# Performance work log

Hardware: AMD Instinct MI355X
Metric: run time of the kernel (lower is better)

Reference implementation:

```python
import jax, jax.numpy as jnp
import numpy as np

GRAPH_SIZES = [864, 1728, 3456, 6912]
VERTEX_NUM = 6890
B, NZ, FC_DIM = 128, 128, 512
CH = [128, 128, 64, 32, 16]
EDGE_FACTOR = 6  # directed edges per node (triangle mesh)
LRELU = 0.2


def setup_inputs() -> dict:
    key = jax.random.key(0)
    ks = jax.random.split(key, 24)
    s = 0.02
    inp = {
        'x': jax.random.normal(ks[0], (B, NZ), jnp.float32),
        'fc_w1': s * jax.random.normal(ks[1], (NZ, FC_DIM), jnp.float32),
        'fc_b1': jnp.zeros((FC_DIM,), jnp.float32),
        'fc_w2': s * jax.random.normal(ks[2], (FC_DIM, GRAPH_SIZES[0] * CH[0]), jnp.float32),
        'fc_b2': jnp.zeros((GRAPH_SIZES[0] * CH[0],), jnp.float32),
    }
    # Chebyshev weights [K=3, C_in, C_out] per layer (+ final conv to 3)
    cio = [(CH[0], CH[1]), (CH[1], CH[2]), (CH[2], CH[3]), (CH[3], CH[4]), (CH[4], 3)]
    for i, (ci, co) in enumerate(cio):
        inp[f'W{i}'] = s * jax.random.normal(ks[3 + i], (3, ci, co), jnp.float32)
        inp[f'b{i}'] = jnp.zeros((co,), jnp.float32)
    # fixed edge lists per level
    for i, n in enumerate(GRAPH_SIZES):
        e = EDGE_FACTOR * n
        inp[f'edge{i}'] = jax.random.randint(ks[10 + i], (2, e), 0, n, dtype=jnp.int64)
    inp['perm_back'] = jax.random.randint(ks[20], (GRAPH_SIZES[-1],), 0, GRAPH_SIZES[-1], dtype=jnp.int64)
    return inp


def cheb_conv(x, edge_index, W, b, num_nodes):
    # PyG-style ChebConv with lambda_max=2: L_hat = L - I = -D^{-1/2} A D^{-1/2}
    src, dst = edge_index[0], edge_index[1]
    deg = jnp.zeros((num_nodes,), x.dtype).at[dst].add(jnp.ones(src.shape, x.dtype))
    dinv = jnp.where(deg > 0, 1.0 / jnp.sqrt(jnp.maximum(deg, 1.0)), 0.0)
    norm = -(dinv[src] * dinv[dst])  # [E]

    def prop(h):  # h: [B, N, C] -> L_hat @ h (gather + scatter-add over edges)
        msg = h[:, src, :] * norm[None, :, None]
        return jnp.zeros_like(h).at[:, dst, :].add(msg)

    Tx0 = x
    Tx1 = prop(Tx0)
    Tx2 = 2.0 * prop(Tx1) - Tx0
    out = (jnp.einsum('bnc,co->bno', Tx0, W[0])
           + jnp.einsum('bnc,co->bno', Tx1, W[1])
           + jnp.einsum('bnc,co->bno', Tx2, W[2]))
    return out + b


def lrelu(x):
    return jnp.where(x >= 0, x, LRELU * x)


def reference(x, fc_w1, fc_b1, fc_w2, fc_b2,
              W0, b0, W1, b1, W2, b2, W3, b3, W4, b4,
              edge0, edge1, edge2, edge3, perm_back):
    h = jax.nn.relu(x @ fc_w1 + fc_b1)
    h = h @ fc_w2 + fc_b2                      # dropout = identity (eval mode)
    h = h.reshape(h.shape[0], GRAPH_SIZES[0], -1)  # [B, 864, 128]
    edges = [edge0, edge1, edge2, edge3]
    Ws = [(W0, b0), (W1, b1), (W2, b2), (W3, b3)]
    for i in range(4):
        h = lrelu(cheb_conv(h, edges[i], Ws[i][0], Ws[i][1], GRAPH_SIZES[i]))
        if i < 3:
            h = jnp.repeat(h, 2, axis=1)       # Upsample(scale_factor=2) along nodes
    h = cheb_conv(h, edge3, W4, b4, GRAPH_SIZES[3])  # final conv to 3 coords
    h = h[:, perm_back, :]                      # perm_data gather
    return h[:, :VERTEX_NUM, :]
```

## Files before the change

### kernel.cpp

```cpp
#include <hip/hip_runtime.h>
#include <hip/hip_bf16.h>

#define DEVFN __device__ __forceinline__

__global__ void k_signal(float* out, float v) {
    if (threadIdx.x == 0 && blockIdx.x == 0) out[0] = v;
}

__global__ void k_detect64(const long long* __restrict__ p, int count, int* flag) {
    if (threadIdx.x == 0 && blockIdx.x == 0) {
        int ok = 1;
        for (int i = 0; i < count; i++) {
            long long v = p[i];
            if (v < 0 || v >= (1LL << 30)) { ok = 0; break; }
        }
        *flag = ok;
    }
}

__global__ __launch_bounds__(256) void k_cvt_idx(const void* __restrict__ p, int n,
                                                 const int* __restrict__ flag,
                                                 int* __restrict__ out) {
    int i = blockIdx.x * 256 + threadIdx.x;
    if (i >= n) return;
    if (*flag) out[i] = (int)((const long long*)p)[i];
    else       out[i] = ((const int*)p)[i];
}

__global__ __launch_bounds__(256) void k_fc1(const float* __restrict__ x,
                                             const float* __restrict__ w,
                                             const float* __restrict__ b,
                                             float* __restrict__ out) {
    int j = blockIdx.x * 256 + threadIdx.x;
    int m = blockIdx.y;
    float acc = b[j];
    const float* xr = x + m * 128;
    for (int k = 0; k < 128; k++)
        acc = fmaf(xr[k], w[k * 512 + j], acc);
    out[m * 512 + j] = fmaxf(acc, 0.f);
}

__global__ __launch_bounds__(256) void k_fc2_gemm3(const float* __restrict__ h1,
                                                   const float* __restrict__ w,
                                                   const float* __restrict__ bias,
                                                   float* __restrict__ out) {
    const int N = 110592, K = 512;
    constexpr int KT = 32, MT = 128, NT = 64, AST = 37;
    __shared__ float At[MT * AST];
    __shared__ float Bt[KT * NT];

    const int tid = threadIdx.x;
    const int cg = tid & 7;
    const int rg = tid >> 3;
    const int nbase = blockIdx.x * NT;
    const int c0 = cg * 8;

    float acc[4][8];
#pragma unroll
    for (int jj = 0; jj < 8; jj++) {
        float bj = bias[nbase + c0 + jj];
#pragma unroll
        for (int r = 0; r < 4; r++) acc[r][jj] = bj;
    }

    for (int k0 = 0; k0 < K; k0 += KT) {
        __syncthreads();
#pragma unroll
        for (int it = 0; it < 4; it++) {
            int idx = tid + it * 256;
            int row = idx >> 3, k4 = (idx & 7) * 4;
            float4 a = *(const float4*)(h1 + row * K + k0 + k4);
            float* dst = At + row * AST + k4;
            dst[0] = a.x; dst[1] = a.y; dst[2] = a.z; dst[3] = a.w;
        }
#pragma unroll
        for (int it = 0; it < 2; it++) {
            int idx = tid + it * 256;
            int kk = idx >> 4, c4 = (idx & 15) * 4;
            *(float4*)(Bt + kk * NT + c4) =
                *(const float4*)(w + (size_t)(k0 + kk) * N + nbase + c4);
        }
        __syncthreads();
#pragma unroll 4
        for (int k = 0; k < KT; k++) {
            float a0 = At[(rg * 4 + 0) * AST + k];
            float a1 = At[(rg * 4 + 1) * AST + k];
            float a2 = At[(rg * 4 + 2) * AST + k];
            float a3 = At[(rg * 4 + 3) * AST + k];
            float4 w0 = *(const float4*)(Bt + k * NT + c0);
            float4 w1 = *(const float4*)(Bt + k * NT + c0 + 4);
            float wv[8] = {w0.x, w0.y, w0.z, w0.w, w1.x, w1.y, w1.z, w1.w};
#pragma unroll
            for (int jj = 0; jj < 8; jj++) {
                acc[0][jj] = fmaf(a0, wv[jj], acc[0][jj]);
                acc[1][jj] = fmaf(a1, wv[jj], acc[1][jj]);
                acc[2][jj] = fmaf(a2, wv[jj], acc[2][jj]);
                acc[3][jj] = fmaf(a3, wv[jj], acc[3][jj]);
            }
        }
    }
#pragma unroll
    for (int r = 0; r < 4; r++) {
        int m = rg * 4 + r;
        float4 o0 = {acc[r][0], acc[r][1], acc[r][2], acc[r][3]};
        float4 o1 = {acc[r][4], acc[r][5], acc[r][6], acc[r][7]};
        *(float4*)(out + (size_t)m * N + nbase + c0) = o0;
        *(float4*)(out + (size_t)m * N + nbase + c0 + 4) = o1;
    }
}

__global__ __launch_bounds__(256) void k_zero_int(int* p, int n) {
    int i = blockIdx.x * 256 + threadIdx.x;
    if (i < n) p[i] = 0;
}

__global__ __launch_bounds__(256) void k_deg(const int* __restrict__ dst, int e,
                                             int* __restrict__ deg) {
    int i = blockIdx.x * 256 + threadIdx.x;
    if (i < e) atomicAdd(&deg[dst[i]], 1);
}

__global__ __launch_bounds__(256) void k_dinv(const int* __restrict__ deg,
                                              float* __restrict__ dinv, int n) {
    int i = blockIdx.x * 256 + threadIdx.x;
    if (i < n) dinv[i] = deg[i] > 0 ? 1.0f / sqrtf((float)deg[i]) : 0.0f;
}

__global__ __launch_bounds__(256) void k_scan(const int* __restrict__ deg,
                                              int* __restrict__ row_ptr, int n) {
    __shared__ int part[256];
    int tid = threadIdx.x;
    int per = (n + 255) / 256;
    int start = tid * per;
    int end = min(start + per, n);
    int s = 0;
    for (int i = start; i < end; i++) s += deg[i];
    part[tid] = s;
    __syncthreads();
    for (int off = 1; off < 256; off <<= 1) {
        int t = (tid >= off) ? part[tid - off] : 0;
        __syncthreads();
        part[tid] += t;
        __syncthreads();
    }
    int base = (tid == 0) ? 0 : part[tid - 1];
    int run = base;
    for (int i = start; i < end; i++) { row_ptr[i] = run; run += deg[i]; }
    if (tid == 255) row_ptr[n] = part[255];
}

__global__ __launch_bounds__(256) void k_fill(const int* __restrict__ src,
                                              const int* __restrict__ dst, int e,
                                              const int* __restrict__ row_ptr,
                                              int* __restrict__ cnt,
                                              const float* __restrict__ dinv,
                                              int* __restrict__ col, float* __restrict__ val) {
    int i = blockIdx.x * 256 + threadIdx.x;
    if (i >= e) return;
    int d = dst[i], s = src[i];
    int slot = row_ptr[d] + atomicAdd(&cnt[d], 1);
    col[slot] = s;
    val[slot] = -dinv[s] * dinv[d];
}

template <int CI, int MODE>
__global__ __launch_bounds__(256) void k_prop2(const float* __restrict__ h,
                                               const float* __restrict__ sub,
                                               const int* __restrict__ row_ptr,
                                               const int* __restrict__ col,
                                               const float* __restrict__ val,
                                               float* __restrict__ out, int n) {
    constexpr int C4 = CI / 4;
    constexpr int BY = 256 / C4;
    int c4 = threadIdx.x;
    int d = blockIdx.x;
    int b = blockIdx.y * BY + threadIdx.y;
    int p0 = row_ptr[d], p1 = row_ptr[d + 1];
    float4 acc = {0.f, 0.f, 0.f, 0.f};
    const float4* hb = (const float4*)h + (size_t)b * n * C4;
    for (int p = p0; p < p1; p++) {
        float vp = val[p];
        float4 hv = hb[(size_t)col[p] * C4 + c4];
        acc.x = fmaf(vp, hv.x, acc.x);
        acc.y = fmaf(vp, hv.y, acc.y);
        acc.z = fmaf(vp, hv.z, acc.z);
        acc.w = fmaf(vp, hv.w, acc.w);
    }
    size_t oi = ((size_t)b * n + d) * C4 + c4;
    if (MODE) {
        float4 s = ((const float4*)sub)[oi];
        acc.x = 2.f * acc.x - s.x;
        acc.y = 2.f * acc.y - s.y;
        acc.z = 2.f * acc.z - s.z;
        acc.w = 2.f * acc.w - s.w;
    }
    ((float4*)out)[oi] = acc;
}

template <int CI>
__global__ __launch_bounds__(256) void k_prop_bc(const float* __restrict__ src,
                                                 const int* __restrict__ row_ptr,
                                                 const int* __restrict__ col,
                                                 const float* __restrict__ val,
                                                 float* __restrict__ out, int n) {
    constexpr int C4 = CI / 4;
    constexpr int BY = 256 / C4;
    int c4 = threadIdx.x;
    int d = blockIdx.x;
    int b = blockIdx.y * BY + threadIdx.y;
    int p0 = row_ptr[d], p1 = row_ptr[d + 1];
    float4 acc = {0.f, 0.f, 0.f, 0.f};
    const float4* hb = (const float4*)src + (size_t)b * (n >> 1) * C4;
    for (int p = p0; p < p1; p++) {
        float vp = val[p];
        float4 hv = hb[(size_t)(col[p] >> 1) * C4 + c4];
        acc.x = fmaf(vp, hv.x, acc.x);
        acc.y = fmaf(vp, hv.y, acc.y);
        acc.z = fmaf(vp, hv.z, acc.z);
        acc.w = fmaf(vp, hv.w, acc.w);
    }
    ((float4*)out)[((size_t)b * n + d) * C4 + c4] = acc;
}

template <int CO>
__global__ __launch_bounds__(256) void k_prop_comb2(const float* __restrict__ pbc,
                                                    const float* __restrict__ a,
                                                    const int* __restrict__ row_ptr,
                                                    const int* __restrict__ col,
                                                    const float* __restrict__ val,
                                                    float* __restrict__ out, int n) {
    constexpr int C4 = CO / 4;
    constexpr int BY = 256 / C4;
    int c4 = threadIdx.x;
    int d = blockIdx.x;
    int b = blockIdx.y * BY + threadIdx.y;
    int p0 = row_ptr[d], p1 = row_ptr[d + 1];
    float4 acc = {0.f, 0.f, 0.f, 0.f};
    const float4* pb4 = (const float4*)pbc + (size_t)b * n * (2 * C4);
    for (int p = p0; p < p1; p++) {
        float vp = val[p];
        float4 hv = pb4[(size_t)col[p] * (2 * C4) + C4 + c4];
        acc.x = fmaf(vp, hv.x, acc.x);
        acc.y = fmaf(vp, hv.y, acc.y);
        acc.z = fmaf(vp, hv.z, acc.z);
        acc.w = fmaf(vp, hv.w, acc.w);
    }
    float4 av = ((const float4*)a)[((size_t)b * (n >> 1) + (d >> 1)) * C4 + c4];
    float4 pbv = pb4[(size_t)d * (2 * C4) + c4];
    float4 f;
    f.x = av.x + pbv.x + 2.f * acc.x;
    f.y = av.y + pbv.y + 2.f * acc.y;
    f.z = av.z + pbv.z + 2.f * acc.z;
    f.w = av.w + pbv.w + 2.f * acc.w;
    f.x = f.x >= 0.f ? f.x : 0.2f * f.x;
    f.y = f.y >= 0.f ? f.y : 0.2f * f.y;
    f.z = f.z >= 0.f ? f.z : 0.2f * f.z;
    f.w = f.w >= 0.f ? f.w : 0.2f * f.w;
    ((float4*)out)[((size_t)b * n + d) * C4 + c4] = f;
}

template <int CI, int CO, bool REPEAT>
__global__ __launch_bounds__(256) void k_cheb_gemm3(const float* __restrict__ t0,
                                                    const float* __restrict__ t1,
                                                    const float* __restrict__ t2,
                                                    const float* __restrict__ W,
                                                    const float* __restrict__ bias,
                                                    float* __restrict__ out, int n) {
    constexpr int CGN = CO / 8;
    constexpr int MT = 1024 / CGN;
    constexpr int KT = 32, AST = 37;
    __shared__ float At[MT * AST];
    __shared__ float Wt_s[KT * CO];

    const int tid = threadIdx.x;
    const int cg = tid % CGN;
    const int rg = tid / CGN;
    const int m_base = blockIdx.x * MT;
    const int c0 = cg * 8;

    float acc[4][8];
#pragma unroll
    for (int jj = 0; jj < 8; jj++) {
        float bj = bias[c0 + jj];
#pragma unroll
        for (int r = 0; r < 4; r++) acc[r][jj] = bj;
    }

    const float* As[3] = {t0, t1, t2};
#pragma unroll 1
    for (int t = 0; t < 3; t++) {
        const float* A = As[t];
        const float* Wg = W + t * CI * CO;
#pragma unroll 1
        for (int k0 = 0; k0 < CI; k0 += KT) {
            __syncthreads();
#pragma unroll
            for (int it = 0; it < MT / 32; it++) {
                int idx = tid + it * 256;
                int row = idx >> 3, k4 = (idx & 7) * 4;
                float4 a = *(const float4*)(A + (size_t)(m_base + row) * CI + k0 + k4);
                float* dst = At + row * AST + k4;
                dst[0] = a.x; dst[1] = a.y; dst[2] = a.z; dst[3] = a.w;
            }
#pragma unroll
            for (int it = 0; it < (KT * CO) / 1024; it++) {
                int idx = tid + it * 256;
                int kk = idx / (CO / 4), c4 = (idx % (CO / 4)) * 4;
                *(float4*)(Wt_s + kk * CO + c4) =
                    *(const float4*)(Wg + (k0 + kk) * CO + c4);
            }
            __syncthreads();
#pragma unroll 4
            for (int k = 0; k < KT; k++) {
                float a0 = At[(rg * 4 + 0) * AST + k];
                float a1 = At[(rg * 4 + 1) * AST + k];
                float a2 = At[(rg * 4 + 2) * AST + k];
                float a3 = At[(rg * 4 + 3) * AST + k];
                float4 w0 = *(const float4*)(Wt_s + k * CO + c0);
                float4 w1 = *(const float4*)(Wt_s + k * CO + c0 + 4);
                float wv[8] = {w0.x, w0.y, w0.z, w0.w, w1.x, w1.y, w1.z, w1.w};
#pragma unroll
                for (int jj = 0; jj < 8; jj++) {
                    acc[0][jj] = fmaf(a0, wv[jj], acc[0][jj]);
                    acc[1][jj] = fmaf(a1, wv[jj], acc[1][jj]);
                    acc[2][jj] = fmaf(a2, wv[jj], acc[2][jj]);
                    acc[3][jj] = fmaf(a3, wv[jj], acc[3][jj]);
                }
            }
        }
    }

#pragma unroll
    for (int r = 0; r < 4; r++) {
        int m = m_base + rg * 4 + r;
#pragma unroll
        for (int jj = 0; jj < 8; jj++) {
            float v = acc[r][jj];
            acc[r][jj] = v >= 0.f ? v : 0.2f * v;
        }
        float4 o0 = {acc[r][0], acc[r][1], acc[r][2], acc[r][3]};
        float4 o1 = {acc[r][4], acc[r][5], acc[r][6], acc[r][7]};
        if (REPEAT) {
            int b = m / n, d = m - (m / n) * n;
            size_t ob = ((size_t)b * (2 * n) + 2 * d) * CO + c0;
            *(float4*)(out + ob) = o0;
            *(float4*)(out + ob + 4) = o1;
            *(float4*)(out + ob + CO) = o0;
            *(float4*)(out + ob + CO + 4) = o1;
        } else {
            *(float4*)(out + (size_t)m * CO + c0) = o0;
            *(float4*)(out + (size_t)m * CO + c0 + 4) = o1;
        }
    }
}

template <int CI, int CO>
__global__ __launch_bounds__(256) void k_cheb_gemmABC(const float* __restrict__ t0,
                                                      const float* __restrict__ W,
                                                      const float* __restrict__ bias,
                                                      float* __restrict__ outA,
                                                      float* __restrict__ outBC) {
    constexpr int CGN = CO / 8;
    constexpr int MT = 1024 / CGN;
    constexpr int KT = 32, AST = 37;
    __shared__ float At[MT * AST];
    __shared__ float Ws[3 * KT * CO];

    const int tid = threadIdx.x;
    const int cg = tid % CGN;
    const int rg = tid / CGN;
    const int m_base = blockIdx.x * MT;
    const int c0 = cg * 8;

    float acc[3][4][8] = {};

#pragma unroll 1
    for (int k0 = 0; k0 < CI; k0 += KT) {
        __syncthreads();
#pragma unroll
        for (int it = 0; it < MT / 32; it++) {
            int idx = tid + it * 256;
            int row = idx >> 3, k4 = (idx & 7) * 4;
            float4 a = *(const float4*)(t0 + (size_t)(m_base + row) * CI + k0 + k4);
            float* dst = At + row * AST + k4;
            dst[0] = a.x; dst[1] = a.y; dst[2] = a.z; dst[3] = a.w;
        }
#pragma unroll
        for (int t = 0; t < 3; t++)
#pragma unroll
            for (int it = 0; it < CO / 32; it++) {
                int idx = tid + it * 256;
                int kk = idx / (CO / 4), c4 = (idx % (CO / 4)) * 4;
                *(float4*)(Ws + t * KT * CO + kk * CO + c4) =
                    *(const float4*)(W + t * CI * CO + (size_t)(k0 + kk) * CO + c4);
            }
        __syncthreads();
#pragma unroll 2
        for (int k = 0; k < KT; k++) {
            float a0 = At[(rg * 4 + 0) * AST + k];
            float a1 = At[(rg * 4 + 1) * AST + k];
            float a2 = At[(rg * 4 + 2) * AST + k];
            float a3 = At[(rg * 4 + 3) * AST + k];
#pragma unroll
            for (int t = 0; t < 3; t++) {
                float4 w0 = *(const float4*)(Ws + t * KT * CO + k * CO + c0);
                float4 w1 = *(const float4*)(Ws + t * KT * CO + k * CO + c0 + 4);
                float wv[8] = {w0.x, w0.y, w0.z, w0.w, w1.x, w1.y, w1.z, w1.w};
#pragma unroll
                for (int jj = 0; jj < 8; jj++) {
                    acc[t][0][jj] = fmaf(a0, wv[jj], acc[t][0][jj]);
                    acc[t][1][jj] = fmaf(a1, wv[jj], acc[t][1][jj]);
                    acc[t][2][jj] = fmaf(a2, wv[jj], acc[t][2][jj]);
                    acc[t][3][jj] = fmaf(a3, wv[jj], acc[t][3][jj]);
                }
            }
        }
    }

#pragma unroll
    for (int r = 0; r < 4; r++) {
        size_t m = m_base + rg * 4 + r;
        float av[8], bv[8], cv[8];
#pragma unroll
        for (int jj = 0; jj < 8; jj++) {
            cv[jj] = acc[2][r][jj];
            av[jj] = acc[0][r][jj] - cv[jj] + bias[c0 + jj];
            bv[jj] = acc[1][r][jj];
        }
        *(float4*)(outA + m * CO + c0)     = (float4){av[0], av[1], av[2], av[3]};
        *(float4*)(outA + m * CO + c0 + 4) = (float4){av[4], av[5], av[6], av[7]};
        float* bc = outBC + m * 2 * CO;
        *(float4*)(bc + c0)          = (float4){bv[0], bv[1], bv[2], bv[3]};
        *(float4*)(bc + c0 + 4)      = (float4){bv[4], bv[5], bv[6], bv[7]};
        *(float4*)(bc + CO + c0)     = (float4){cv[0], cv[1], cv[2], cv[3]};
        *(float4*)(bc + CO + c0 + 4) = (float4){cv[4], cv[5], cv[6], cv[7]};
    }
}

__global__ __launch_bounds__(256) void k_cheb_smallABC(const float* __restrict__ t0,
                                                       const float* __restrict__ W,
                                                       const float* __restrict__ bias,
                                                       float* __restrict__ outA,
                                                       float* __restrict__ outBC) {
    constexpr int CI = 32, CO = 16, MT = 256, AST = 33;
    __shared__ float At[MT * AST];
    __shared__ float Ws[3 * CI * CO];

    const int tid = threadIdx.x;
    const int cg = tid & 1;
    const int rg = tid >> 1;
    const int c0 = cg * 8;
    const int m_base = blockIdx.x * MT;

    for (int i = tid; i < 384; i += 256)
        ((float4*)Ws)[i] = ((const float4*)W)[i];

#pragma unroll
    for (int it = 0; it < 8; it++) {
        int idx = tid + it * 256;
        int row = idx >> 3, k4 = (idx & 7) * 4;
        float4 a = *(const float4*)(t0 + (size_t)(m_base + row) * CI + k4);
        float* dst = At + row * AST + k4;
        dst[0] = a.x; dst[1] = a.y; dst[2] = a.z; dst[3] = a.w;
    }
    __syncthreads();

    float acc[3][2][8] = {};
#pragma unroll 4
    for (int k = 0; k < CI; k++) {
        float a0 = At[rg * AST + k];
        float a1 = At[(rg + 128) * AST + k];
#pragma unroll
        for (int t = 0; t < 3; t++) {
            float4 w0 = *(const float4*)(Ws + t * CI * CO + k * CO + c0);
            float4 w1 = *(const float4*)(Ws + t * CI * CO + k * CO + c0 + 4);
            float wv[8] = {w0.x, w0.y, w0.z, w0.w, w1.x, w1.y, w1.z, w1.w};
#pragma unroll
            for (int jj = 0; jj < 8; jj++) {
                acc[t][0][jj] = fmaf(a0, wv[jj], acc[t][0][jj]);
                acc[t][1][jj] = fmaf(a1, wv[jj], acc[t][1][jj]);
            }
        }
    }

#pragma unroll
    for (int r = 0; r < 2; r++) {
        size_t m = m_base + rg + r * 128;
        float av[8], bv[8], cv[8];
#pragma unroll
        for (int jj = 0; jj < 8; jj++) {
            cv[jj] = acc[2][r][jj];
            av[jj] = acc[0][r][jj] - cv[jj] + bias[c0 + jj];
            bv[jj] = acc[1][r][jj];
        }
        *(float4*)(outA + m * CO + c0)     = (float4){av[0], av[1], av[2], av[3]};
        *(float4*)(outA + m * CO + c0 + 4) = (float4){av[4], av[5], av[6], av[7]};
        float* bc = outBC + m * 2 * CO;
        *(float4*)(bc + c0)          = (float4){bv[0], bv[1], bv[2], bv[3]};
        *(float4*)(bc + c0 + 4)      = (float4){bv[4], bv[5], bv[6], bv[7]};
        *(float4*)(bc + CO + c0)     = (float4){cv[0], cv[1], cv[2], cv[3]};
        *(float4*)(bc + CO + c0 + 4) = (float4){cv[4], cv[5], cv[6], cv[7]};
    }
}

__global__ __launch_bounds__(256) void k_final_conv(const float* __restrict__ t0,
                                                    const float* __restrict__ t1,
                                                    const float* __restrict__ t2,
                                                    const float* __restrict__ W,
                                                    const float* __restrict__ bias,
                                                    float* __restrict__ out, int M) {
    int m = blockIdx.x * 256 + threadIdx.x;
    if (m >= M) return;
    float a0 = bias[0], a1 = bias[1], a2 = bias[2];
    const float* hs[3] = {t0, t1, t2};
#pragma unroll
    for (int t = 0; t < 3; t++) {
        const float4* h4 = (const float4*)(hs[t] + (size_t)m * 16);
        const float* Wt = W + t * 48;
#pragma unroll
        for (int q = 0; q < 4; q++) {
            float4 hv = h4[q];
            const float* Wq = Wt + q * 12;
            a0 = fmaf(hv.x, Wq[0], a0); a1 = fmaf(hv.x, Wq[1], a1); a2 = fmaf(hv.x, Wq[2], a2);
            a0 = fmaf(hv.y, Wq[3], a0); a1 = fmaf(hv.y, Wq[4], a1); a2 = fmaf(hv.y, Wq[5], a2);
            a0 = fmaf(hv.z, Wq[6], a0); a1 = fmaf(hv.z, Wq[7], a1); a2 = fmaf(hv.z, Wq[8], a2);
            a0 = fmaf(hv.w, Wq[9], a0); a1 = fmaf(hv.w, Wq[10], a1); a2 = fmaf(hv.w, Wq[11], a2);
        }
    }
    out[(size_t)m * 3 + 0] = a0;
    out[(size_t)m * 3 + 1] = a1;
    out[(size_t)m * 3 + 2] = a2;
}

__global__ __launch_bounds__(256) void k_permute(const float* __restrict__ h,
                                                 const int* __restrict__ perm,
                                                 float* __restrict__ out) {
    const int V = 6890, N = 6912;
    int idx = blockIdx.x * 256 + threadIdx.x;
    if (idx >= 128 * V * 3) return;
    int c = idx % 3;
    int t = idx / 3;
    int v = t % V;
    int b = t / V;
    int p = perm[v];
    out[idx] = h[((size_t)b * N + p) * 3 + c];
}

extern "C" void kernel_launch(void* const* d_in, const int* in_sizes, int n_in,
                              void* d_out, int out_size, void* d_ws, size_t ws_size,
                              hipStream_t stream) {
    float* out = (float*)d_out;

    static const int SIZES[20] = {
        16384, 65536, 512, 56623104, 110592,
        49152, 128, 24576, 64, 6144, 32, 1536, 16, 144, 3,
        10368, 20736, 41472, 82944, 6912
    };
    const void* in[20];
    bool map_ok = (n_in == 20);
    if (map_ok) {
        for (int s = 0; s < 20; s++) {
            int found = -1;
            for (int i = 0; i < n_in; i++)
                if (in_sizes[i] == SIZES[s]) { found = i; break; }
            if (found < 0) { map_ok = false; break; }
            in[s] = d_in[found];
        }
    }
    if (!map_ok)
        for (int i = 0; i < 20 && i < n_in; i++) in[i] = d_in[i];

    const float* x     = (const float*)in[0];
    const float* fc_w1 = (const float*)in[1];
    const float* fc_b1 = (const float*)in[2];
    const float* fc_w2 = (const float*)in[3];
    const float* fc_b2 = (const float*)in[4];
    const float* W0 = (const float*)in[5];
    const float* b0 = (const float*)in[6];
    const float* W1 = (const float*)in[7];
    const float* b1 = (const float*)in[8];
    const float* W2 = (const float*)in[9];
    const float* b2 = (const float*)in[10];
    const float* W3 = (const float*)in[11];
    const float* b3 = (const float*)in[12];
    const float* W4 = (const float*)in[13];
    const float* b4 = (const float*)in[14];

    const size_t SZ = 28311552;
    float* ws = (float*)d_ws;
    float* buf0 = ws;
    float* buf1 = ws + SZ;
    float* buf2 = ws + 2 * SZ;
    float* buf3 = ws + 3 * SZ;
    float* h1   = ws + 4 * SZ;
    float* dinv = h1 + 65536;
    float* val  = dinv + 6912;
    int* ideg = (int*)(val + 41472);
    int* rowp = ideg + 6912;
    int* cnt  = rowp + 6913;
    int* col  = cnt + 6912;
    int* e0 = col + 41472;
    int* e1 = e0 + 10368;
    int* e2 = e1 + 20736;
    int* e3 = e2 + 41472;
    int* pm = e3 + 82944;
    int* flag = pm + 6912;
    size_t needed = (char*)(flag + 1) - (char*)d_ws;
    if (ws_size < needed) {
        k_signal<<<1, 64, 0, stream>>>(out, 1000.0f);
        return;
    }

    k_detect64<<<1, 64, 0, stream>>>((const long long*)in[15], 64, flag);
    k_cvt_idx<<<(10368 + 255) / 256, 256, 0, stream>>>(in[15], 10368, flag, e0);
    k_cvt_idx<<<(20736 + 255) / 256, 256, 0, stream>>>(in[16], 20736, flag, e1);
    k_cvt_idx<<<(41472 + 255) / 256, 256, 0, stream>>>(in[17], 41472, flag, e2);
    k_cvt_idx<<<(82944 + 255) / 256, 256, 0, stream>>>(in[18], 82944, flag, e3);
    k_cvt_idx<<<(6912 + 255) / 256, 256, 0, stream>>>(in[19], 6912, flag, pm);

    k_fc1<<<dim3(2, 128), 256, 0, stream>>>(x, fc_w1, fc_b1, h1);
    k_fc2_gemm3<<<1728, 256, 0, stream>>>(h1, fc_w2, fc_b2, buf0);

    auto build = [&](const int* edge, int e, int n) {
        int nb_n = (n + 255) / 256, nb_e = (e + 255) / 256;
        k_zero_int<<<nb_n, 256, 0, stream>>>(ideg, n);
        k_zero_int<<<nb_n, 256, 0, stream>>>(cnt, n);
        k_deg<<<nb_e, 256, 0, stream>>>(edge + e, e, ideg);
        k_dinv<<<nb_n, 256, 0, stream>>>(ideg, dinv, n);
        k_scan<<<1, 256, 0, stream>>>(ideg, rowp, n);
        k_fill<<<nb_e, 256, 0, stream>>>(edge, edge + e, e, rowp, cnt, dinv, col, val);
    };

    build(e0, 6 * 864, 864);
    k_prop2<128, 0><<<dim3(864, 16), dim3(32, 8), 0, stream>>>(buf0, buf0, rowp, col, val, buf1, 864);
    k_prop2<128, 1><<<dim3(864, 16), dim3(32, 8), 0, stream>>>(buf1, buf0, rowp, col, val, buf2, 864);
    k_cheb_gemm3<128, 128, false><<<1728, 256, 0, stream>>>(buf0, buf1, buf2, W0, b0, buf3, 864);

    build(e1, 6 * 1728, 1728);
    k_cheb_gemmABC<128, 64><<<864, 256, 0, stream>>>(buf3, W1, b1, buf1, buf2);
    k_prop_bc<128><<<dim3(1728, 16), dim3(32, 8), 0, stream>>>(buf2, rowp, col, val, buf0, 1728);
    k_prop_comb2<64><<<dim3(1728, 8), dim3(16, 16), 0, stream>>>(buf0, buf1, rowp, col, val, buf3, 1728);

    build(e2, 6 * 3456, 3456);
    k_cheb_gemmABC<64, 32><<<864, 256, 0, stream>>>(buf3, W2, b2, buf1, buf2);
    k_prop_bc<64><<<dim3(3456, 8), dim3(16, 16), 0, stream>>>(buf2, rowp, col, val, buf0, 3456);
    k_prop_comb2<32><<<dim3(3456, 4), dim3(8, 32), 0, stream>>>(buf0, buf1, rowp, col, val, buf3, 3456);

    build(e3, 6 * 6912, 6912);
    k_cheb_smallABC<<<1728, 256, 0, stream>>>(buf3, W3, b3, buf1, buf2);
    k_prop_bc<32><<<dim3(6912, 4), dim3(8, 32), 0, stream>>>(buf2, rowp, col, val, buf0, 6912);
    k_prop_comb2<16><<<dim3(6912, 2), dim3(4, 64), 0, stream>>>(buf0, buf1, rowp, col, val, buf3, 6912);

    k_prop2<16, 0><<<dim3(6912, 2), dim3(4, 64), 0, stream>>>(buf3, buf3, rowp, col, val, buf1, 6912);
    k_prop2<16, 1><<<dim3(6912, 2), dim3(4, 64), 0, stream>>>(buf1, buf3, rowp, col, val, buf2, 6912);
    k_final_conv<<<(884736 + 255) / 256, 256, 0, stream>>>(buf3, buf1, buf2, W4, b4, buf0, 884736);

    int tot = 128 * 6890 * 3;
    k_permute<<<(tot + 255) / 256, 256, 0, stream>>>(buf0, pm, out);

    if (!map_ok) k_signal<<<1, 64, 0, stream>>>(out, 2000.0f);
}
```

Measured before the change: 1.729 ms.

## Project final conv to 3 channels before propagation and fuse permute into combine

```diff
diff --git a/kernel.cpp b/kernel.cpp
--- a/kernel.cpp
+++ b/kernel.cpp
@@ -503,47 +503,71 @@
     }
 }
 
-__global__ __launch_bounds__(256) void k_final_conv(const float* __restrict__ t0,
-                                                    const float* __restrict__ t1,
-                                                    const float* __restrict__ t2,
-                                                    const float* __restrict__ W,
-                                                    const float* __restrict__ bias,
-                                                    float* __restrict__ out, int M) {
-    int m = blockIdx.x * 256 + threadIdx.x;
+__global__ __launch_bounds__(256) void k_final_ABC(const float* __restrict__ h,
+                                                   const float* __restrict__ W,
+                                                   const float* __restrict__ bias,
+                                                   float* __restrict__ outA,
+                                                   float* __restrict__ outBC, int M) {
+    __shared__ float Ws[144];
+    int tid = threadIdx.x;
+    if (tid < 144) Ws[tid] = W[tid];
+    __syncthreads();
+    int m = blockIdx.x * 256 + tid;
     if (m >= M) return;
-    float a0 = bias[0], a1 = bias[1], a2 = bias[2];
-    const float* hs[3] = {t0, t1, t2};
-#pragma unroll
-    for (int t = 0; t < 3; t++) {
-        const float4* h4 = (const float4*)(hs[t] + (size_t)m * 16);
-        const float* Wt = W + t * 48;
-#pragma unroll
-        for (int q = 0; q < 4; q++) {
-            float4 hv = h4[q];
-            const float* Wq = Wt + q * 12;
-            a0 = fmaf(hv.x, Wq[0], a0); a1 = fmaf(hv.x, Wq[1], a1); a2 = fmaf(hv.x, Wq[2], a2);
-            a0 = fmaf(hv.y, Wq[3], a0); a1 = fmaf(hv.y, Wq[4], a1); a2 = fmaf(hv.y, Wq[5], a2);
-            a0 = fmaf(hv.z, Wq[6], a0); a1 = fmaf(hv.z, Wq[7], a1); a2 = fmaf(hv.z, Wq[8], a2);
-            a0 = fmaf(hv.w, Wq[9], a0); a1 = fmaf(hv.w, Wq[10], a1); a2 = fmaf(hv.w, Wq[11], a2);
-        }
-    }
-    out[(size_t)m * 3 + 0] = a0;
-    out[(size_t)m * 3 + 1] = a1;
-    out[(size_t)m * 3 + 2] = a2;
-}
-
-__global__ __launch_bounds__(256) void k_permute(const float* __restrict__ h,
-                                                 const int* __restrict__ perm,
-                                                 float* __restrict__ out) {
+    const float4* h4 = (const float4*)(h + (size_t)m * 16);
+    float hv[16];
+#pragma unroll
+    for (int q = 0; q < 4; q++) {
+        float4 v = h4[q];
+        hv[q * 4 + 0] = v.x; hv[q * 4 + 1] = v.y; hv[q * 4 + 2] = v.z; hv[q * 4 + 3] = v.w;
+    }
+    float t0a[3] = {0.f, 0.f, 0.f}, bv[3] = {0.f, 0.f, 0.f}, cv[3] = {0.f, 0.f, 0.f};
+#pragma unroll
+    for (int k = 0; k < 16; k++) {
+        float x = hv[k];
+#pragma unroll
+        for (int c = 0; c < 3; c++) {
+            t0a[c] = fmaf(x, Ws[k * 3 + c], t0a[c]);
+            bv[c]  = fmaf(x, Ws[48 + k * 3 + c], bv[c]);
+            cv[c]  = fmaf(x, Ws[96 + k * 3 + c], cv[c]);
+        }
+    }
+    float4 av = {t0a[0] - cv[0] + bias[0], t0a[1] - cv[1] + bias[1],
+                 t0a[2] - cv[2] + bias[2], 0.f};
+    ((float4*)outA)[m] = av;
+    float4* bc = (float4*)(outBC + (size_t)m * 8);
+    bc[0] = (float4){bv[0], bv[1], bv[2], 0.f};
+    bc[1] = (float4){cv[0], cv[1], cv[2], 0.f};
+}
+
+__global__ __launch_bounds__(256) void k_final_comb(const float* __restrict__ pbc,
+                                                    const float* __restrict__ a,
+                                                    const int* __restrict__ row_ptr,
+                                                    const int* __restrict__ col,
+                                                    const float* __restrict__ val,
+                                                    const int* __restrict__ perm,
+                                                    float* __restrict__ out) {
     const int V = 6890, N = 6912;
     int idx = blockIdx.x * 256 + threadIdx.x;
-    if (idx >= 128 * V * 3) return;
-    int c = idx % 3;
-    int t = idx / 3;
-    int v = t % V;
-    int b = t / V;
-    int p = perm[v];
-    out[idx] = h[((size_t)b * N + p) * 3 + c];
+    if (idx >= 128 * V) return;
+    int v = idx % V;
+    int b = idx / V;
+    int d = perm[v];
+    int p0 = row_ptr[d], p1 = row_ptr[d + 1];
+    const float4* pb4 = (const float4*)pbc + (size_t)b * N * 2;
+    float ax = 0.f, ay = 0.f, az = 0.f;
+    for (int p = p0; p < p1; p++) {
+        float vp = val[p];
+        float4 pc = pb4[(size_t)col[p] * 2 + 1];
+        ax = fmaf(vp, pc.x, ax);
+        ay = fmaf(vp, pc.y, ay);
+        az = fmaf(vp, pc.z, az);
+    }
+    float4 av = ((const float4*)a)[(size_t)b * N + d];
+    float4 pbv = pb4[(size_t)d * 2];
+    out[(size_t)idx * 3 + 0] = av.x + pbv.x + 2.f * ax;
+    out[(size_t)idx * 3 + 1] = av.y + pbv.y + 2.f * ay;
+    out[(size_t)idx * 3 + 2] = av.z + pbv.z + 2.f * az;
 }
 
 extern "C" void kernel_launch(void* const* d_in, const int* in_sizes, int n_in,
@@ -651,12 +675,9 @@
     k_prop_bc<32><<<dim3(6912, 4), dim3(8, 32), 0, stream>>>(buf2, rowp, col, val, buf0, 6912);
     k_prop_comb2<16><<<dim3(6912, 2), dim3(4, 64), 0, stream>>>(buf0, buf1, rowp, col, val, buf3, 6912);
 
-    k_prop2<16, 0><<<dim3(6912, 2), dim3(4, 64), 0, stream>>>(buf3, buf3, rowp, col, val, buf1, 6912);
-    k_prop2<16, 1><<<dim3(6912, 2), dim3(4, 64), 0, stream>>>(buf1, buf3, rowp, col, val, buf2, 6912);
-    k_final_conv<<<(884736 + 255) / 256, 256, 0, stream>>>(buf3, buf1, buf2, W4, b4, buf0, 884736);
-
-    int tot = 128 * 6890 * 3;
-    k_permute<<<(tot + 255) / 256, 256, 0, stream>>>(buf0, pm, out);
+    k_final_ABC<<<(884736 + 255) / 256, 256, 0, stream>>>(buf3, W4, b4, buf1, buf2, 884736);
+    k_prop2<8, 0><<<dim3(6912, 1), dim3(2, 128), 0, stream>>>(buf2, buf2, rowp, col, val, buf0, 6912);
+    k_final_comb<<<(128 * 6890 + 255) / 256, 256, 0, stream>>>(buf0, buf1, rowp, col, val, pm, out);
 
     if (!map_ok) k_signal<<<1, 64, 0, stream>>>(out, 2000.0f);
 }
```

Result: no change. 1.705 ms (-1.4%).
